# Optimization experiments

Measured on AMD Instinct MI355X. Metric: run time of the kernel, lower is better.

Reference implementation:

```python
import jax, jax.numpy as jnp
import numpy as np

NUM_CLASSES = 100
CLUSTERS_PER_CLASS = 64
LATENT_DIM = 128
BATCH = 32768


def setup_inputs() -> dict:
    key = jax.random.key(0)
    kx, kc, kl = jax.random.split(key, 3)
    x = jax.random.normal(kx, (BATCH, LATENT_DIM), dtype=jnp.float32)
    # nn.Parameter(torch.randn(C, Kc, D) * 0.1)
    centers = jax.random.normal(kc, (NUM_CLASSES, CLUSTERS_PER_CLASS, LATENT_DIM), dtype=jnp.float32) * 0.1
    labels = jax.random.randint(kl, (BATCH,), 0, NUM_CLASSES, dtype=jnp.int64)
    return {"x": x, "centers": centers, "labels": labels}


def reference(x, centers, labels):
    # [C, Kc, D] -> [K, D]
    all_centers = centers.reshape(-1, LATENT_DIM).astype(x.dtype)
    x2 = jnp.sum(x * x, axis=-1, keepdims=True)            # [B,1]
    c2 = jnp.sum(all_centers * all_centers, axis=-1)       # [K]
    sq = x2 + c2[None, :] - 2.0 * jnp.einsum('bd,kd->bk', x, all_centers)
    distances = jnp.sqrt(jnp.maximum(sq, 0.0))             # [B,K]
    closest_indices = jnp.argmin(distances, axis=1)        # [B]
    class_predictions = closest_indices // CLUSTERS_PER_CLASS
    cluster_assignments = closest_indices % CLUSTERS_PER_CLASS
    quantized_hard = all_centers[closest_indices]          # [B,D]
    min_distances = jnp.take_along_axis(distances, closest_indices[:, None], axis=1)[:, 0]
    # straight-through estimator (training path in the torch module)
    quantized = x + jax.lax.stop_gradient(quantized_hard - x)
    return quantized, cluster_assignments, min_distances, class_predictions
```

## Files before the change

### kernel.cpp

```cpp
#include <hip/hip_runtime.h>
#include <math.h>

#define BATCH  32768
#define D      128
#define K      6400
#define KC     64
#define ROWS_PER_BLOCK 64
#define CHUNK_C 128
#define NCHUNK (K / CHUNK_C)

typedef _Float16 half8 __attribute__((ext_vector_type(8)));
typedef float    floatx4 __attribute__((ext_vector_type(4)));

typedef __attribute__((address_space(3))) unsigned       lds_uint;
typedef __attribute__((address_space(1))) const unsigned glb_uint;

__device__ __forceinline__ void async_lds16(const void* g, void* l) {
    __builtin_amdgcn_global_load_lds((glb_uint*)g, (lds_uint*)l, 16, 0, 0);
}

__global__ __launch_bounds__(256) void pack_kernel(const float* __restrict__ centers,
                                                   _Float16* __restrict__ wh,
                                                   float* __restrict__ c2n) {
    int tid = blockIdx.x * 256 + threadIdx.x;
    int ch = tid >> 11;
    int u  = (tid >> 7) & 15;
    int cw = tid & 127;
    int center = ch * CHUNK_C + cw;
    const float* src = centers + (size_t)center * D + u * 8;
    float4 a = *(const float4*)src;
    float4 b = *(const float4*)(src + 4);
    float f[8] = {a.x, a.y, a.z, a.w, b.x, b.y, b.z, b.w};
    half8 h;
#pragma unroll
    for (int j = 0; j < 8; ++j) h[j] = (_Float16)f[j];
    *(half8*)(wh + (size_t)tid * 8) = h;

    if (blockIdx.x < K / KC) {
        int c_local = threadIdx.x >> 2, part = threadIdx.x & 3;
        int c = blockIdx.x * 64 + c_local;
        const float4* p = (const float4*)(centers + (size_t)c * D + part * 32);
        float s = 0.f;
#pragma unroll
        for (int i = 0; i < 8; ++i) {
            float4 v = p[i];
            s = fmaf(v.x, v.x, s); s = fmaf(v.y, v.y, s);
            s = fmaf(v.z, v.z, s); s = fmaf(v.w, v.w, s);
        }
        s += __shfl_xor(s, 1, 64);
        s += __shfl_xor(s, 2, 64);
        if (part == 0) c2n[c] = -0.5f * s;
    }
}

__global__ __launch_bounds__(256, 2) void dist_kernel(
    const float* __restrict__ x, const float* __restrict__ centers,
    const _Float16* __restrict__ wh, const float* __restrict__ c2n,
    float* __restrict__ out) {
    __shared__ char lds[32768];

    const int t    = threadIdx.x;
    const int w    = t >> 6;
    const int L    = t & 63;
    const int quad = L >> 4;
    const int n16  = L & 15;
    const int rowhalf = w & 1;
    const int chalf   = w >> 1;
    const int gr0  = blockIdx.x * ROWS_PER_BLOCK;

    half8 Ah[2][4];
#pragma unroll
    for (int rt = 0; rt < 2; ++rt) {
        int r = gr0 + rowhalf * 32 + rt * 16 + n16;
        const float* xr = x + (size_t)r * D + quad * 8;
#pragma unroll
        for (int ks = 0; ks < 4; ++ks) {
            float4 a = *(const float4*)(xr + ks * 32);
            float4 b = *(const float4*)(xr + ks * 32 + 4);
            float f[8] = {a.x, a.y, a.z, a.w, b.x, b.y, b.z, b.w};
            half8 h;
#pragma unroll
            for (int j = 0; j < 8; ++j) h[j] = (_Float16)f[j];
            Ah[rt][ks] = h;
        }
    }

    float b1[8], b2[8];
    int   j1_[8], j2_[8];
#pragma unroll
    for (int k = 0; k < 8; ++k) { b1[k] = -3.4e38f; b2[k] = -3.4e38f; j1_[k] = 0; j2_[k] = 0; }

    for (int ch = 0; ch < NCHUNK; ++ch) {
        __syncthreads();
        const char* gh = (const char*)wh + (size_t)ch * 32768;
#pragma unroll
        for (int i = 0; i < 8; ++i) {
            int seg = w + i * 4;
            async_lds16(gh + seg * 1024 + L * 16, lds + seg * 1024);
        }
        const int kbase = ch * CHUNK_C + chalf * 64;
        float c2v[4];
#pragma unroll
        for (int ct = 0; ct < 4; ++ct) c2v[ct] = c2n[kbase + ct * 16 + n16];
        __syncthreads();

        floatx4 acc[2][4];
#pragma unroll
        for (int rt = 0; rt < 2; ++rt)
#pragma unroll
            for (int ct = 0; ct < 4; ++ct)
                acc[rt][ct] = (floatx4){c2v[ct], c2v[ct], c2v[ct], c2v[ct]};

#pragma unroll
        for (int ks = 0; ks < 4; ++ks) {
            const half8* pb = (const half8*)lds + (ks * 4 + quad) * 128 + chalf * 64 + n16;
#pragma unroll
            for (int ct = 0; ct < 4; ++ct) {
                half8 Bf = pb[ct * 16];
                acc[0][ct] = __builtin_amdgcn_mfma_f32_16x16x32_f16(Ah[0][ks], Bf, acc[0][ct], 0, 0, 0);
                acc[1][ct] = __builtin_amdgcn_mfma_f32_16x16x32_f16(Ah[1][ks], Bf, acc[1][ct], 0, 0, 0);
            }
        }

        int i0 = kbase + n16;
#pragma unroll
        for (int rt = 0; rt < 2; ++rt)
#pragma unroll
            for (int reg = 0; reg < 4; ++reg) {
                float s0 = acc[rt][0][reg], s1 = acc[rt][1][reg];
                float s2 = acc[rt][2][reg], s3 = acc[rt][3][reg];
                bool g01 = s1 > s0, g23 = s3 > s2;
                float m01 = g01 ? s1 : s0;  int x01 = g01 ? i0 + 16 : i0;
                float m23 = g23 ? s3 : s2;  int x23 = g23 ? i0 + 48 : i0 + 32;
                bool gq = m23 > m01;
                float q  = gq ? m23 : m01;  int qi = gq ? x23 : x01;
                int k = rt * 4 + reg;
                bool bet1 = q > b1[k];
                bool bet2 = q > b2[k];
                float nb2 = bet1 ? b1[k] : (bet2 ? q : b2[k]);
                int   nj2 = bet1 ? j1_[k] : (bet2 ? qi : j2_[k]);
                b1[k]  = bet1 ? q : b1[k];
                j1_[k] = bet1 ? qi : j1_[k];
                b2[k]  = nb2;
                j2_[k] = nj2;
            }
    }

    __syncthreads();
    int* candL = (int*)lds;

#pragma unroll
    for (int k = 0; k < 8; ++k) {
        float v1 = b1[k], v2 = b2[k];
        int   p1 = j1_[k], p2 = j2_[k];
#pragma unroll
        for (int m = 1; m < 8; m <<= 1) {
            float o1 = __shfl_xor(v1, m, 64), o2 = __shfl_xor(v2, m, 64);
            int   q1 = __shfl_xor(p1, m, 64), q2 = __shfl_xor(p2, m, 64);
            bool firstMine = (v1 > o1) || (v1 == o1 && p1 < q1);
            float nv1 = firstMine ? v1 : o1;  int np1 = firstMine ? p1 : q1;
            float cb  = firstMine ? o1 : v1;  int cpi = firstMine ? q1 : p1;
            float ob  = firstMine ? v2 : o2;  int obi = firstMine ? p2 : q2;
            bool secOwn = (ob > cb) || (ob == cb && obi < cpi);
            v1 = nv1; p1 = np1;
            v2 = secOwn ? ob : cb;  p2 = secOwn ? obi : cpi;
        }
        if ((n16 & 7) == 0) {
            int rloc = rowhalf * 32 + (k >> 2) * 16 + quad * 4 + (k & 3);
            int g = chalf * 2 + (n16 >> 3);
            candL[rloc * 8 + g * 2 + 0] = p1;
            candL[rloc * 8 + g * 2 + 1] = p2;
        }
    }
    __syncthreads();

    float* out_q   = out;
    float* out_clu = out + (size_t)BATCH * D;
    float* out_md  = out_clu + BATCH;
    float* out_cls = out_md + BATCH;

    {
        int r = t >> 2, p = t & 3;
        int ixa = candL[r * 8 + p * 2 + 0];
        int ixb = candL[r * 8 + p * 2 + 1];
        const float4* xr4 = (const float4*)(x + (size_t)(gr0 + r) * D);
        const float4* ca4 = (const float4*)(centers + (size_t)ixa * D);
        const float4* cb4 = (const float4*)(centers + (size_t)ixb * D);
        float dota = 0.f, dotb = 0.f, x2s = 0.f, c2a = 0.f, c2b = 0.f;
#pragma unroll
        for (int d4 = 0; d4 < 32; ++d4) {
            float4 xv = xr4[d4], av = ca4[d4], bv = cb4[d4];
            dota = fmaf(xv.x, av.x, dota); dota = fmaf(xv.y, av.y, dota);
            dota = fmaf(xv.z, av.z, dota); dota = fmaf(xv.w, av.w, dota);
            dotb = fmaf(xv.x, bv.x, dotb); dotb = fmaf(xv.y, bv.y, dotb);
            dotb = fmaf(xv.z, bv.z, dotb); dotb = fmaf(xv.w, bv.w, dotb);
            x2s = fmaf(xv.x, xv.x, x2s); x2s = fmaf(xv.y, xv.y, x2s);
            x2s = fmaf(xv.z, xv.z, x2s); x2s = fmaf(xv.w, xv.w, x2s);
            c2a = fmaf(av.x, av.x, c2a); c2a = fmaf(av.y, av.y, c2a);
            c2a = fmaf(av.z, av.z, c2a); c2a = fmaf(av.w, av.w, c2a);
            c2b = fmaf(bv.x, bv.x, c2b); c2b = fmaf(bv.y, bv.y, c2b);
            c2b = fmaf(bv.z, bv.z, c2b); c2b = fmaf(bv.w, bv.w, c2b);
        }
        float sqa = x2s + c2a - 2.f * dota;
        float sqb = x2s + c2b - 2.f * dotb;
        bool aw = (sqa < sqb) || (sqa == sqb && ixa < ixb);
        float sq = aw ? sqa : sqb;
        int   ix = aw ? ixa : ixb;
#pragma unroll
        for (int m = 1; m < 4; m <<= 1) {
            float osq = __shfl_xor(sq, m, 64);
            int   oix = __shfl_xor(ix, m, 64);
            if (osq < sq || (osq == sq && oix < ix)) { sq = osq; ix = oix; }
        }
        int* winL = (int*)(lds + 16384);
        if (p == 0) {
            out_md[gr0 + r]  = sqrtf(fmaxf(sq, 0.f));
            out_clu[gr0 + r] = (float)(ix & (KC - 1));
            out_cls[gr0 + r] = (float)(ix >> 6);
            winL[r] = ix;
        }
    }
    __syncthreads();

    {
        const int* winL = (const int*)(lds + 16384);
        const float4* cg4 = (const float4*)centers;
        const float4* xg4 = (const float4*)x + (size_t)gr0 * 32;
        float4* oq4 = (float4*)out_q + (size_t)gr0 * 32;
#pragma unroll
        for (int p = 0; p < 8; ++p) {
            int lin = p * 256 + t;
            int r = lin >> 5, d4 = lin & 31;
            int ix = winL[r];
            float4 cv = cg4[(size_t)ix * 32 + d4];
            float4 xv = xg4[lin];
            float4 o;
            o.x = xv.x + (cv.x - xv.x);
            o.y = xv.y + (cv.y - xv.y);
            o.z = xv.z + (cv.z - xv.z);
            o.w = xv.w + (cv.w - xv.w);
            oq4[lin] = o;
        }
    }
}

extern "C" void kernel_launch(void* const* d_in, const int* in_sizes, int n_in,
                              void* d_out, int out_size, void* d_ws, size_t ws_size,
                              hipStream_t stream) {
    const float* x       = (const float*)d_in[0];
    const float* centers = (const float*)d_in[1];
    float* out = (float*)d_out;

    _Float16* wh  = (_Float16*)d_ws;
    float*    c2n = (float*)(wh + (size_t)K * D);

    pack_kernel<<<(K * 16) / 256, 256, 0, stream>>>(centers, wh, c2n);
    dist_kernel<<<BATCH / ROWS_PER_BLOCK, 256, 0, stream>>>(x, centers, wh, c2n, out);
}
```

Baseline: 197.7 us.

## Split center range across two grid halves and merge results in a final kernel

The distance kernel now launches a 2D grid in which each block scans only half of the 6400 centers, doubling the block count to 1024. Launch bounds are raised to 4 blocks per SM. Per-half best squared distance and index go to workspace, and a new final kernel picks the better half and writes distances, labels and the quantized output. This is meant to improve occupancy and load balance across CUs. The cost is loading and converting each x row twice, an extra kernel launch, and a workspace round trip.

```diff
diff --git a/kernel.cpp b/kernel.cpp
--- a/kernel.cpp
+++ b/kernel.cpp
@@ -7,7 +7,8 @@
 #define KC     64
 #define ROWS_PER_BLOCK 64
 #define CHUNK_C 128
-#define NCHUNK (K / CHUNK_C)
+#define HALVES 2
+#define CHUNKS_PER_HALF 25
 
 typedef _Float16 half8 __attribute__((ext_vector_type(8)));
 typedef float    floatx4 __attribute__((ext_vector_type(4)));
@@ -53,10 +54,10 @@
     }
 }
 
-__global__ __launch_bounds__(256, 2) void dist_kernel(
+__global__ __launch_bounds__(256, 4) void dist_kernel(
     const float* __restrict__ x, const float* __restrict__ centers,
     const _Float16* __restrict__ wh, const float* __restrict__ c2n,
-    float* __restrict__ out) {
+    float* __restrict__ ws_sq, int* __restrict__ ws_ix) {
     __shared__ char lds[32768];
 
     const int t    = threadIdx.x;
@@ -66,6 +67,7 @@
     const int n16  = L & 15;
     const int rowhalf = w & 1;
     const int chalf   = w >> 1;
+    const int half = blockIdx.y;
     const int gr0  = blockIdx.x * ROWS_PER_BLOCK;
 
     half8 Ah[2][4];
@@ -90,19 +92,21 @@
 #pragma unroll
     for (int k = 0; k < 8; ++k) { b1[k] = -3.4e38f; b2[k] = -3.4e38f; j1_[k] = 0; j2_[k] = 0; }
 
-    for (int ch = 0; ch < NCHUNK; ++ch) {
+    const char* gh = (const char*)wh + (size_t)half * CHUNKS_PER_HALF * 32768;
+
+    for (int ch = 0; ch < CHUNKS_PER_HALF; ++ch) {
         __syncthreads();
-        const char* gh = (const char*)wh + (size_t)ch * 32768;
 #pragma unroll
         for (int i = 0; i < 8; ++i) {
             int seg = w + i * 4;
             async_lds16(gh + seg * 1024 + L * 16, lds + seg * 1024);
         }
-        const int kbase = ch * CHUNK_C + chalf * 64;
+        const int kbase = (half * CHUNKS_PER_HALF + ch) * CHUNK_C + chalf * 64;
         float c2v[4];
 #pragma unroll
         for (int ct = 0; ct < 4; ++ct) c2v[ct] = c2n[kbase + ct * 16 + n16];
         __syncthreads();
+        gh += 32768;
 
         floatx4 acc[2][4];
 #pragma unroll
@@ -174,11 +178,6 @@
     }
     __syncthreads();
 
-    float* out_q   = out;
-    float* out_clu = out + (size_t)BATCH * D;
-    float* out_md  = out_clu + BATCH;
-    float* out_cls = out_md + BATCH;
-
     {
         int r = t >> 2, p = t & 3;
         int ixa = candL[r * 8 + p * 2 + 0];
@@ -212,36 +211,43 @@
             int   oix = __shfl_xor(ix, m, 64);
             if (osq < sq || (osq == sq && oix < ix)) { sq = osq; ix = oix; }
         }
-        int* winL = (int*)(lds + 16384);
         if (p == 0) {
-            out_md[gr0 + r]  = sqrtf(fmaxf(sq, 0.f));
-            out_clu[gr0 + r] = (float)(ix & (KC - 1));
-            out_cls[gr0 + r] = (float)(ix >> 6);
-            winL[r] = ix;
-        }
-    }
-    __syncthreads();
-
-    {
-        const int* winL = (const int*)(lds + 16384);
-        const float4* cg4 = (const float4*)centers;
-        const float4* xg4 = (const float4*)x + (size_t)gr0 * 32;
-        float4* oq4 = (float4*)out_q + (size_t)gr0 * 32;
-#pragma unroll
-        for (int p = 0; p < 8; ++p) {
-            int lin = p * 256 + t;
-            int r = lin >> 5, d4 = lin & 31;
-            int ix = winL[r];
-            float4 cv = cg4[(size_t)ix * 32 + d4];
-            float4 xv = xg4[lin];
-            float4 o;
-            o.x = xv.x + (cv.x - xv.x);
-            o.y = xv.y + (cv.y - xv.y);
-            o.z = xv.z + (cv.z - xv.z);
-            o.w = xv.w + (cv.w - xv.w);
-            oq4[lin] = o;
-        }
-    }
+            ws_sq[(size_t)half * BATCH + gr0 + r] = sq;
+            ws_ix[(size_t)half * BATCH + gr0 + r] = ix;
+        }
+    }
+}
+
+__global__ __launch_bounds__(256) void final_kernel(
+    const float* __restrict__ x, const float* __restrict__ centers,
+    const float* __restrict__ ws_sq, const int* __restrict__ ws_ix,
+    float* __restrict__ out) {
+    int g = blockIdx.x * 256 + threadIdx.x;
+    int row = g >> 5, d4 = g & 31;
+
+    float sqa = ws_sq[row],         sqb = ws_sq[BATCH + row];
+    int   ixa = ws_ix[row],         ixb = ws_ix[BATCH + row];
+    bool aw = (sqa <= sqb);
+    float sq = aw ? sqa : sqb;
+    int   ix = aw ? ixa : ixb;
+
+    float* out_clu = out + (size_t)BATCH * D;
+    float* out_md  = out_clu + BATCH;
+    float* out_cls = out_md + BATCH;
+    if (d4 == 0) {
+        out_md[row]  = sqrtf(fmaxf(sq, 0.f));
+        out_clu[row] = (float)(ix & (KC - 1));
+        out_cls[row] = (float)(ix >> 6);
+    }
+
+    float4 cv = ((const float4*)centers)[(size_t)ix * 32 + d4];
+    float4 xv = ((const float4*)x)[(size_t)row * 32 + d4];
+    float4 o;
+    o.x = xv.x + (cv.x - xv.x);
+    o.y = xv.y + (cv.y - xv.y);
+    o.z = xv.z + (cv.z - xv.z);
+    o.w = xv.w + (cv.w - xv.w);
+    ((float4*)out)[(size_t)row * 32 + d4] = o;
 }
 
 extern "C" void kernel_launch(void* const* d_in, const int* in_sizes, int n_in,
@@ -251,9 +257,13 @@
     const float* centers = (const float*)d_in[1];
     float* out = (float*)d_out;
 
-    _Float16* wh  = (_Float16*)d_ws;
-    float*    c2n = (float*)(wh + (size_t)K * D);
+    _Float16* wh    = (_Float16*)d_ws;
+    float*    c2n   = (float*)(wh + (size_t)K * D);
+    float*    ws_sq = c2n + K;
+    int*      ws_ix = (int*)(ws_sq + HALVES * BATCH);
 
     pack_kernel<<<(K * 16) / 256, 256, 0, stream>>>(centers, wh, c2n);
-    dist_kernel<<<BATCH / ROWS_PER_BLOCK, 256, 0, stream>>>(x, centers, wh, c2n, out);
-}
+    dim3 grid(BATCH / ROWS_PER_BLOCK, HALVES);
+    dist_kernel<<<grid, 256, 0, stream>>>(x, centers, wh, c2n, ws_sq, ws_ix);
+    final_kernel<<<(BATCH * 32) / 256, 256, 0, stream>>>(x, centers, ws_sq, ws_ix, out);
+}
```

Measured after the change: 204.3 us. 1.03x slower.

## Split centers across waves and load B fragments directly from global memory

Applied to the files above, without the earlier changes.

The LDS-staged, block-synchronised chunk loop is replaced by a scheme where each of four wave-pairs in a 512-thread block scans its own quarter of the centers (25 groups of 64), reading packed fp16 B fragments straight from global/L2. The per-chunk barriers and the async global-to-LDS copies go away. The candidate reduction widens to 8 candidates per row pair, which adds a little refinement work. In exchange, each wave now streams B from cache with no sharing through LDS, which raises L2/VMEM traffic and exposes load latency that must be hidden by occupancy.

```diff
diff --git a/kernel.cpp b/kernel.cpp
--- a/kernel.cpp
+++ b/kernel.cpp
@@ -6,27 +6,19 @@
 #define K      6400
 #define KC     64
 #define ROWS_PER_BLOCK 64
-#define CHUNK_C 128
-#define NCHUNK (K / CHUNK_C)
+#define GROUPS_PER_WAVE 25
 
 typedef _Float16 half8 __attribute__((ext_vector_type(8)));
 typedef float    floatx4 __attribute__((ext_vector_type(4)));
-
-typedef __attribute__((address_space(3))) unsigned       lds_uint;
-typedef __attribute__((address_space(1))) const unsigned glb_uint;
-
-__device__ __forceinline__ void async_lds16(const void* g, void* l) {
-    __builtin_amdgcn_global_load_lds((glb_uint*)g, (lds_uint*)l, 16, 0, 0);
-}
 
 __global__ __launch_bounds__(256) void pack_kernel(const float* __restrict__ centers,
                                                    _Float16* __restrict__ wh,
                                                    float* __restrict__ c2n) {
     int tid = blockIdx.x * 256 + threadIdx.x;
-    int ch = tid >> 11;
-    int u  = (tid >> 7) & 15;
-    int cw = tid & 127;
-    int center = ch * CHUNK_C + cw;
+    int g  = tid >> 10;
+    int u  = (tid >> 6) & 15;
+    int cw = tid & 63;
+    int center = g * 64 + cw;
     const float* src = centers + (size_t)center * D + u * 8;
     float4 a = *(const float4*)src;
     float4 b = *(const float4*)(src + 4);
@@ -53,11 +45,12 @@
     }
 }
 
-__global__ __launch_bounds__(256, 2) void dist_kernel(
+__global__ __launch_bounds__(512, 4) void dist_kernel(
     const float* __restrict__ x, const float* __restrict__ centers,
     const _Float16* __restrict__ wh, const float* __restrict__ c2n,
     float* __restrict__ out) {
-    __shared__ char lds[32768];
+    __shared__ int candL[ROWS_PER_BLOCK * 16];
+    __shared__ int winL[ROWS_PER_BLOCK];
 
     const int t    = threadIdx.x;
     const int w    = t >> 6;
@@ -65,7 +58,7 @@
     const int quad = L >> 4;
     const int n16  = L & 15;
     const int rowhalf = w & 1;
-    const int chalf   = w >> 1;
+    const int q       = w >> 1;
     const int gr0  = blockIdx.x * ROWS_PER_BLOCK;
 
     half8 Ah[2][4];
@@ -90,64 +83,58 @@
 #pragma unroll
     for (int k = 0; k < 8; ++k) { b1[k] = -3.4e38f; b2[k] = -3.4e38f; j1_[k] = 0; j2_[k] = 0; }
 
-    for (int ch = 0; ch < NCHUNK; ++ch) {
-        __syncthreads();
-        const char* gh = (const char*)wh + (size_t)ch * 32768;
-#pragma unroll
-        for (int i = 0; i < 8; ++i) {
-            int seg = w + i * 4;
-            async_lds16(gh + seg * 1024 + L * 16, lds + seg * 1024);
-        }
-        const int kbase = ch * CHUNK_C + chalf * 64;
+    const half8* pw = (const half8*)wh + ((size_t)q * GROUPS_PER_WAVE) * 1024 + quad * 64 + n16;
+    const float* pc = c2n + q * GROUPS_PER_WAVE * 64 + n16;
+
+    for (int ci = 0; ci < GROUPS_PER_WAVE; ++ci) {
+        floatx4 acc[2][4];
+#pragma unroll
+        for (int rt = 0; rt < 2; ++rt)
+#pragma unroll
+            for (int ct = 0; ct < 4; ++ct) acc[rt][ct] = (floatx4){0.f, 0.f, 0.f, 0.f};
+
         float c2v[4];
 #pragma unroll
-        for (int ct = 0; ct < 4; ++ct) c2v[ct] = c2n[kbase + ct * 16 + n16];
-        __syncthreads();
-
-        floatx4 acc[2][4];
+        for (int ct = 0; ct < 4; ++ct) c2v[ct] = pc[ci * 64 + ct * 16];
+
+        const half8* pg = pw + ci * 1024;
+#pragma unroll
+        for (int ks = 0; ks < 4; ++ks) {
+            half8 Bf[4];
+#pragma unroll
+            for (int ct = 0; ct < 4; ++ct) Bf[ct] = pg[ks * 256 + ct * 16];
+#pragma unroll
+            for (int ct = 0; ct < 4; ++ct) {
+                acc[0][ct] = __builtin_amdgcn_mfma_f32_16x16x32_f16(Ah[0][ks], Bf[ct], acc[0][ct], 0, 0, 0);
+                acc[1][ct] = __builtin_amdgcn_mfma_f32_16x16x32_f16(Ah[1][ks], Bf[ct], acc[1][ct], 0, 0, 0);
+            }
+        }
+
+        int i0 = (q * GROUPS_PER_WAVE + ci) * 64 + n16;
 #pragma unroll
         for (int rt = 0; rt < 2; ++rt)
 #pragma unroll
-            for (int ct = 0; ct < 4; ++ct)
-                acc[rt][ct] = (floatx4){c2v[ct], c2v[ct], c2v[ct], c2v[ct]};
-
-#pragma unroll
-        for (int ks = 0; ks < 4; ++ks) {
-            const half8* pb = (const half8*)lds + (ks * 4 + quad) * 128 + chalf * 64 + n16;
-#pragma unroll
-            for (int ct = 0; ct < 4; ++ct) {
-                half8 Bf = pb[ct * 16];
-                acc[0][ct] = __builtin_amdgcn_mfma_f32_16x16x32_f16(Ah[0][ks], Bf, acc[0][ct], 0, 0, 0);
-                acc[1][ct] = __builtin_amdgcn_mfma_f32_16x16x32_f16(Ah[1][ks], Bf, acc[1][ct], 0, 0, 0);
-            }
-        }
-
-        int i0 = kbase + n16;
-#pragma unroll
-        for (int rt = 0; rt < 2; ++rt)
-#pragma unroll
             for (int reg = 0; reg < 4; ++reg) {
-                float s0 = acc[rt][0][reg], s1 = acc[rt][1][reg];
-                float s2 = acc[rt][2][reg], s3 = acc[rt][3][reg];
+                float s0 = acc[rt][0][reg] + c2v[0];
+                float s1 = acc[rt][1][reg] + c2v[1];
+                float s2 = acc[rt][2][reg] + c2v[2];
+                float s3 = acc[rt][3][reg] + c2v[3];
                 bool g01 = s1 > s0, g23 = s3 > s2;
                 float m01 = g01 ? s1 : s0;  int x01 = g01 ? i0 + 16 : i0;
                 float m23 = g23 ? s3 : s2;  int x23 = g23 ? i0 + 48 : i0 + 32;
                 bool gq = m23 > m01;
-                float q  = gq ? m23 : m01;  int qi = gq ? x23 : x01;
+                float v  = gq ? m23 : m01;  int vi = gq ? x23 : x01;
                 int k = rt * 4 + reg;
-                bool bet1 = q > b1[k];
-                bool bet2 = q > b2[k];
-                float nb2 = bet1 ? b1[k] : (bet2 ? q : b2[k]);
-                int   nj2 = bet1 ? j1_[k] : (bet2 ? qi : j2_[k]);
-                b1[k]  = bet1 ? q : b1[k];
-                j1_[k] = bet1 ? qi : j1_[k];
+                bool bet1 = v > b1[k];
+                bool bet2 = v > b2[k];
+                float nb2 = bet1 ? b1[k] : (bet2 ? v : b2[k]);
+                int   nj2 = bet1 ? j1_[k] : (bet2 ? vi : j2_[k]);
+                b1[k]  = bet1 ? v : b1[k];
+                j1_[k] = bet1 ? vi : j1_[k];
                 b2[k]  = nb2;
                 j2_[k] = nj2;
             }
     }
-
-    __syncthreads();
-    int* candL = (int*)lds;
 
 #pragma unroll
     for (int k = 0; k < 8; ++k) {
@@ -167,9 +154,9 @@
         }
         if ((n16 & 7) == 0) {
             int rloc = rowhalf * 32 + (k >> 2) * 16 + quad * 4 + (k & 3);
-            int g = chalf * 2 + (n16 >> 3);
-            candL[rloc * 8 + g * 2 + 0] = p1;
-            candL[rloc * 8 + g * 2 + 1] = p2;
+            int col = q * 4 + (n16 >> 3) * 2;
+            candL[rloc * 16 + col + 0] = p1;
+            candL[rloc * 16 + col + 1] = p2;
         }
     }
     __syncthreads();
@@ -180,9 +167,9 @@
     float* out_cls = out_md + BATCH;
 
     {
-        int r = t >> 2, p = t & 3;
-        int ixa = candL[r * 8 + p * 2 + 0];
-        int ixb = candL[r * 8 + p * 2 + 1];
+        int r = t >> 3, p = t & 7;
+        int ixa = candL[r * 16 + p * 2 + 0];
+        int ixb = candL[r * 16 + p * 2 + 1];
         const float4* xr4 = (const float4*)(x + (size_t)(gr0 + r) * D);
         const float4* ca4 = (const float4*)(centers + (size_t)ixa * D);
         const float4* cb4 = (const float4*)(centers + (size_t)ixb * D);
@@ -207,12 +194,11 @@
         float sq = aw ? sqa : sqb;
         int   ix = aw ? ixa : ixb;
 #pragma unroll
-        for (int m = 1; m < 4; m <<= 1) {
+        for (int m = 1; m < 8; m <<= 1) {
             float osq = __shfl_xor(sq, m, 64);
             int   oix = __shfl_xor(ix, m, 64);
             if (osq < sq || (osq == sq && oix < ix)) { sq = osq; ix = oix; }
         }
-        int* winL = (int*)(lds + 16384);
         if (p == 0) {
             out_md[gr0 + r]  = sqrtf(fmaxf(sq, 0.f));
             out_clu[gr0 + r] = (float)(ix & (KC - 1));
@@ -223,13 +209,12 @@
     __syncthreads();
 
     {
-        const int* winL = (const int*)(lds + 16384);
         const float4* cg4 = (const float4*)centers;
         const float4* xg4 = (const float4*)x + (size_t)gr0 * 32;
         float4* oq4 = (float4*)out_q + (size_t)gr0 * 32;
 #pragma unroll
-        for (int p = 0; p < 8; ++p) {
-            int lin = p * 256 + t;
+        for (int p = 0; p < 4; ++p) {
+            int lin = p * 512 + t;
             int r = lin >> 5, d4 = lin & 31;
             int ix = winL[r];
             float4 cv = cg4[(size_t)ix * 32 + d4];
@@ -255,5 +240,5 @@
     float*    c2n = (float*)(wh + (size_t)K * D);
 
     pack_kernel<<<(K * 16) / 256, 256, 0, stream>>>(centers, wh, c2n);
-    dist_kernel<<<BATCH / ROWS_PER_BLOCK, 256, 0, stream>>>(x, centers, wh, c2n, out);
+    dist_kernel<<<BATCH / ROWS_PER_BLOCK, 512, 0, stream>>>(x, centers, wh, c2n, out);
 }
```

Result: slower. 210.6 us (+6.5%).
